# Kernel tuning notes

Measured on AMD Instinct MI355X. Metric: run time of the kernel, lower is better.

## Reference

```python
import jax, jax.numpy as jnp
import numpy as np

N = 16384          # tokens
D_IN = 512         # input_dim
D_OUT = 512        # output_dim
H = 256            # expert hidden
E = 10             # num_experts
TOP_K = 2


def setup_inputs() -> dict:
    key = jax.random.key(0)
    ks = jax.random.split(key, 12)
    s_in = 1.0 / np.sqrt(D_IN)
    s_h = 1.0 / np.sqrt(H)
    s_o = 1.0 / np.sqrt(D_OUT)
    return {
        "x": jax.random.normal(ks[0], (N, D_IN), dtype=jnp.float32),
        "gate_w": jax.random.uniform(ks[1], (D_IN, E), minval=-s_in, maxval=s_in),
        "gate_b": jax.random.uniform(ks[2], (E,), minval=-s_in, maxval=s_in),
        "w1": jax.random.uniform(ks[3], (E, D_IN, H), minval=-s_in, maxval=s_in),
        "b1": jax.random.uniform(ks[4], (E, H), minval=-s_in, maxval=s_in),
        "w2": jax.random.uniform(ks[5], (E, H, D_OUT), minval=-s_h, maxval=s_h),
        "b2": jax.random.uniform(ks[6], (E, D_OUT), minval=-s_h, maxval=s_h),
        "cls_w": jax.random.uniform(ks[7], (D_OUT, D_OUT), minval=-s_o, maxval=s_o),
        "cls_b": jax.random.uniform(ks[8], (D_OUT,), minval=-s_o, maxval=s_o),
        "vec_w": jax.random.uniform(ks[9], (D_OUT, D_OUT), minval=-s_o, maxval=s_o),
        "vec_b": jax.random.uniform(ks[10], (D_OUT,), minval=-s_o, maxval=s_o),
    }


def reference(x, gate_w, gate_b, w1, b1, w2, b2, cls_w, cls_b, vec_w, vec_b):
    # Gating: softmax over experts, take top-k, renormalize
    gate_probs = jax.nn.softmax(x @ gate_w + gate_b, axis=-1)          # [N, E]
    top_v, top_i = jax.lax.top_k(gate_probs, TOP_K)                    # [N, K]
    top_v = top_v / jnp.sum(top_v, axis=-1, keepdims=True)
    # Scatter renormalized top-k probs into dense per-expert weights [N, E]
    n_idx = jnp.arange(x.shape[0])[:, None]
    w = jnp.zeros_like(gate_probs).at[n_idx, top_i].add(top_v)
    # Expert MLPs (vectorized over experts; zero weight == not dispatched)
    h = jax.nn.relu(jnp.einsum("nd,edh->neh", x, w1) + b1)             # [N, E, H]
    y = jnp.einsum("neh,eho->neo", h, w2) + b2                          # [N, E, Dout]
    combined = jnp.einsum("neo,ne->no", y, w)                           # [N, Dout]
    cls_out = combined @ cls_w + cls_b
    vec_out = combined @ vec_w + vec_b
    return (cls_out, vec_out)
```

## Files before the change

kernel.cpp:

```cpp
#include <hip/hip_runtime.h>

#define NTOK 16384
#define DIN  512
#define DOUT 512
#define HDIM 256
#define NEXP 10
#define NSLOT (2*NTOK)
#define NSEG  (2*NEXP)
#define BM 128
#define BN 128
#define BK 64

typedef unsigned short u16;
typedef unsigned int   u32;
typedef short s16x8 __attribute__((ext_vector_type(8)));
typedef float f32x4 __attribute__((ext_vector_type(4)));

__device__ __forceinline__ u16 f2b(float f){
  union { float f; u32 u; } c; c.f = f;
  u32 r = c.u + 0x7FFFu + ((c.u >> 16) & 1u);
  return (u16)(r >> 16);
}
__device__ __forceinline__ float b2f(u16 v){
  union { u32 u; float f; } c; c.u = ((u32)v) << 16; return c.f;
}
__device__ __forceinline__ u32 pk2(float lo, float hi){
  u32 r;
  asm("v_cvt_pk_bf16_f32 %0, %1, %2" : "=v"(r) : "v"(lo), "v"(hi));
  return r;
}
__device__ __forceinline__ s16x8 cvt8(const float* p){
  f32x4 a = *(const f32x4*)p;
  f32x4 b = *(const f32x4*)(p + 4);
  union { u32 u[4]; s16x8 v; } c;
  c.u[0] = pk2(a[0], a[1]); c.u[1] = pk2(a[2], a[3]);
  c.u[2] = pk2(b[0], b[1]); c.u[3] = pk2(b[2], b[3]);
  return c.v;
}

__global__ __launch_bounds__(64) void k_zero(int* counts){
  if (threadIdx.x < NSEG) counts[threadIdx.x] = 0;
}

__global__ __launch_bounds__(256) void k_gate(
    const float* __restrict__ x, const float* __restrict__ gw, const float* __restrict__ gb,
    int* __restrict__ tke, float* __restrict__ tkw, int* __restrict__ counts)
{
  __shared__ int cnt[NSEG];
  __shared__ __align__(16) float xs[16*512];
  __shared__ __align__(16) float lgw[5120];
  const int tid = threadIdx.x;
  if (tid < NSEG) cnt[tid] = 0;
  for (int d = tid; d < 512; d += 256){
    float g[10];
    #pragma unroll
    for (int r = 0; r < 10; ++r) g[r] = gw[d*10 + r];
    #pragma unroll
    for (int p = 0; p < 5; ++p){
      lgw[(p*512 + d)*2    ] = g[2*p];
      lgw[(p*512 + d)*2 + 1] = g[2*p+1];
    }
  }
  const float* xsrc = x + (size_t)blockIdx.x * 16 * 512;
  #pragma unroll
  for (int q = 0; q < 8; ++q){
    int i = tid + q*256;
    *(f32x4*)&xs[i*4] = *(const f32x4*)&xsrc[i*4];
  }
  __syncthreads();

  const int wave = tid >> 6, lane = tid & 63;
  #pragma unroll
  for (int tt = 0; tt < 4; ++tt){
    const int lt = wave*4 + tt;
    const int token = blockIdx.x*16 + lt;
    float acc[NEXP];
    #pragma unroll
    for (int e = 0; e < NEXP; ++e) acc[e] = 0.f;
    #pragma unroll
    for (int dd = 0; dd < 8; ++dd){
      int d = dd*64 + lane;
      float xv = xs[lt*512 + d];
      #pragma unroll
      for (int p = 0; p < 5; ++p){
        float2 g2 = *(const float2*)&lgw[(p*512 + d)*2];
        acc[2*p]   += xv * g2.x;
        acc[2*p+1] += xv * g2.y;
      }
    }
    #pragma unroll
    for (int e = 0; e < NEXP; ++e){
      #pragma unroll
      for (int off = 32; off > 0; off >>= 1) acc[e] += __shfl_xor(acc[e], off, 64);
    }
    if (lane == 0){
      float l[NEXP];
      #pragma unroll
      for (int e = 0; e < NEXP; ++e) l[e] = acc[e] + gb[e];
      int bi = 0; float bv = l[0];
      #pragma unroll
      for (int e = 1; e < NEXP; ++e) if (l[e] > bv){ bv = l[e]; bi = e; }
      int si = -1; float sv = -1e30f;
      #pragma unroll
      for (int e = 0; e < NEXP; ++e) if (e != bi && l[e] > sv){ sv = l[e]; si = e; }
      float w0 = 1.f / (1.f + expf(sv - bv));
      tke[2*token]   = bi;  tke[2*token+1] = si;
      tkw[2*token]   = w0;  tkw[2*token+1] = 1.f - w0;
      atomicAdd(&cnt[2*bi], 1);  atomicAdd(&cnt[2*si+1], 1);
    }
  }
  __syncthreads();
  if (tid < NSEG && cnt[tid] > 0)
    atomicAdd(&counts[tid], cnt[tid]);
}

__global__ __launch_bounds__(64) void k_scan(
    const int* __restrict__ counts, int* __restrict__ offsets, int* __restrict__ cursors)
{
  if (threadIdx.x == 0){
    int s = 0;
    for (int i = 0; i < NSEG; ++i){ offsets[i] = s; s += counts[i]; }
    offsets[NSEG] = s;
  }
  if (threadIdx.x < NSEG) cursors[threadIdx.x] = 0;
}

__global__ __launch_bounds__(256) void k_scatter(
    const int* __restrict__ tke, const float* __restrict__ tkw,
    const int* __restrict__ offsets, int* __restrict__ cursors,
    int* __restrict__ tok_slot, float* __restrict__ w_slot)
{
  __shared__ int lcnt[NSEG], lbase[NSEG];
  if (threadIdx.x < NSEG) lcnt[threadIdx.x] = 0;
  __syncthreads();
  int n = blockIdx.x * 256 + threadIdx.x;
  int g0 = 2*tke[2*n], g1 = 2*tke[2*n+1] + 1;
  int p0 = atomicAdd(&lcnt[g0], 1);
  int p1 = atomicAdd(&lcnt[g1], 1);
  __syncthreads();
  if (threadIdx.x < NSEG) lbase[threadIdx.x] = atomicAdd(&cursors[threadIdx.x], lcnt[threadIdx.x]);
  __syncthreads();
  int s0 = offsets[g0] + lbase[g0] + p0;
  int s1 = offsets[g1] + lbase[g1] + p1;
  tok_slot[s0] = n; w_slot[s0] = tkw[2*n];
  tok_slot[s1] = n; w_slot[s1] = tkw[2*n+1];
}

__global__ __launch_bounds__(256) void k_wt(
    const float* __restrict__ in, u16* __restrict__ out, int R, int C)
{
  __shared__ float tile[32][33];
  const float* src = in + (size_t)blockIdx.z * R * C;
  u16* dst = out + (size_t)blockIdx.z * R * C;
  int cb = blockIdx.x * 32, rb = blockIdx.y * 32;
  int tx = threadIdx.x & 31, ty = threadIdx.x >> 5;
  #pragma unroll
  for (int i = 0; i < 4; ++i)
    tile[ty + i*8][tx] = src[(size_t)(rb + ty + i*8) * C + cb + tx];
  __syncthreads();
  #pragma unroll
  for (int i = 0; i < 4; ++i)
    dst[(size_t)(cb + ty + i*8) * R + rb + tx] = f2b(tile[tx][ty + i*8]);
}

__global__ __launch_bounds__(256) void k_wtt(
    const float* __restrict__ W, u16* __restrict__ out)
{
  int gid = blockIdx.x * 256 + threadIdx.x;
  int c16 = gid & 15;
  int kc  = (gid >> 4) & 63;
  int cg  = gid >> 10;
  int col = cg*16 + c16;
  s16x8 v;
  #pragma unroll
  for (int q = 0; q < 8; ++q)
    v[q] = (short)f2b(W[(size_t)(kc*8 + q) * DOUT + col]);
  *(s16x8*)(out + (size_t)gid * 8) = v;
}

__global__ __launch_bounds__(256, 2) void k_h(
    const float* __restrict__ x, const u16* __restrict__ w1tb, const float* __restrict__ b1,
    const int* __restrict__ offsets, const int* __restrict__ tok_slot,
    u16* __restrict__ h)
{
  __shared__ __align__(16) char pool[65536];
  u16* As = (u16*)pool;
  u16* Bs = (u16*)(pool + 32768);
  __shared__ int toks[BM];
  const int e   = blockIdx.z;
  const int off = offsets[2*e];
  const int cnt = offsets[2*e+2] - off;
  const int c0  = blockIdx.x * BM;
  if (c0 >= cnt) return;
  const int n0  = blockIdx.y * BN;
  const int tid = threadIdx.x;

  if (tid < BM){
    int r = c0 + tid;
    toks[tid] = tok_slot[off + (r < cnt ? r : cnt - 1)];
  }
  __syncthreads();

  const u16* Bg = w1tb + ((size_t)e * HDIM + n0) * DIN;

  int crow[4], ckk[4];
  #pragma unroll
  for (int i = 0; i < 4; ++i){
    int c = tid + i*256;
    crow[i] = c >> 3; ckk[i] = (c & 7) * 8;
  }
  int tokr[4];
  #pragma unroll
  for (int i = 0; i < 4; ++i) tokr[i] = toks[crow[i]];

  s16x8 ra[4], rb[4];
  auto loadregs = [&](int ks){
    #pragma unroll
    for (int i = 0; i < 4; ++i){
      ra[i] = cvt8(x + (size_t)tokr[i]*DIN + ks*BK + ckk[i]);
      rb[i] = *(const s16x8*)(Bg + (size_t)crow[i]*DIN + ks*BK + ckk[i]);
    }
  };
  auto writeregs = [&](int buf){
    #pragma unroll
    for (int i = 0; i < 4; ++i){
      u32 byt = (u32)((crow[i]*BK + ckk[i])*2) ^ ((u32)(crow[i]&7)<<4);
      *(s16x8*)((char*)As + buf*16384 + byt) = ra[i];
      *(s16x8*)((char*)Bs + buf*16384 + byt) = rb[i];
    }
  };

  const int wv = tid >> 6, lane = tid & 63;
  const int lr = lane & 15, lk = lane >> 4;
  const int wr = (wv >> 1) * 64, wc = (wv & 1) * 64;

  f32x4 acc[4][4];
  #pragma unroll
  for (int i = 0; i < 4; ++i)
    #pragma unroll
    for (int j = 0; j < 4; ++j) acc[i][j] = (f32x4){0.f,0.f,0.f,0.f};

  loadregs(0); writeregs(0);
  int cur = 0;
  const int NK = DIN / BK;
  for (int ks = 0; ks < NK; ++ks){
    __syncthreads();
    if (ks + 1 < NK) loadregs(ks + 1);
    #pragma unroll
    for (int sub = 0; sub < 2; ++sub){
      s16x8 af[4], bf[4];
      #pragma unroll
      for (int g = 0; g < 4; ++g){
        int arow = wr + g*16 + lr;
        u32 ab = (u32)((arow*BK + sub*32 + lk*8)*2) ^ ((u32)(arow&7)<<4);
        af[g] = *(const s16x8*)((char*)As + cur*16384 + ab);
        int bcol = wc + g*16 + lr;
        u32 bb = (u32)((bcol*BK + sub*32 + lk*8)*2) ^ ((u32)(bcol&7)<<4);
        bf[g] = *(const s16x8*)((char*)Bs + cur*16384 + bb);
      }
      #pragma unroll
      for (int i = 0; i < 4; ++i)
        #pragma unroll
        for (int j = 0; j < 4; ++j)
          acc[i][j] = __builtin_amdgcn_mfma_f32_16x16x32_bf16(af[i], bf[j], acc[i][j], 0, 0, 0);
    }
    if (ks + 1 < NK) writeregs(cur ^ 1);
    cur ^= 1;
  }
  __syncthreads();

  u16* outh = (u16*)pool;
  #pragma unroll
  for (int j = 0; j < 4; ++j){
    int col = wc + j*16 + lr;
    float bias = b1[e*HDIM + n0 + col];
    #pragma unroll
    for (int i = 0; i < 4; ++i)
      #pragma unroll
      for (int r = 0; r < 4; ++r){
        int row = wr + i*16 + lk*4 + r;
        float v = acc[i][j][r] + bias;
        outh[row*136 + col] = f2b(v > 0.f ? v : 0.f);
      }
  }
  __syncthreads();
  {
    int r = tid >> 1, half = tid & 1;
    if (c0 + r < cnt){
      u16* dst = h + (size_t)(off + c0 + r) * HDIM + n0 + half*64;
      const u16* src = outh + r*136 + half*64;
      #pragma unroll
      for (int q = 0; q < 8; ++q)
        *(s16x8*)(dst + q*8) = *(const s16x8*)(src + q*8);
    }
  }
}

template<int PASS>
__global__ __launch_bounds__(256, 2) void k_y(
    const u16* __restrict__ h, const u16* __restrict__ w2tb, const float* __restrict__ b2,
    const int* __restrict__ offsets, const int* __restrict__ tok_slot,
    const float* __restrict__ w_slot, u16* __restrict__ cmb)
{
  __shared__ __align__(16) char pool[67584];
  u16* As = (u16*)pool;
  u16* Bs = (u16*)(pool + 32768);
  __shared__ int   toks[BM];
  __shared__ float wts[BM];
  const int e    = blockIdx.z;
  const int segb = offsets[2*e + PASS];
  const int segc = offsets[2*e + PASS + 1] - segb;
  const int c0   = blockIdx.x * BM;
  if (c0 >= segc) return;
  const int n0   = blockIdx.y * BN;
  const int tid  = threadIdx.x;

  if (tid < BM){
    int r = c0 + tid;
    int s = segb + (r < segc ? r : segc - 1);
    toks[tid] = tok_slot[s];
    wts[tid]  = w_slot[s];
  }

  const u16* Ag = h + (size_t)(segb + c0) * HDIM;
  const u16* Bg = w2tb + ((size_t)e * DOUT + n0) * HDIM;

  int crow[4], ckk[4];
  #pragma unroll
  for (int i = 0; i < 4; ++i){
    int c = tid + i*256;
    crow[i] = c >> 3; ckk[i] = (c & 7) * 8;
  }
  s16x8 ra[4], rb[4];
  auto loadregs = [&](int ks){
    #pragma unroll
    for (int i = 0; i < 4; ++i){
      ra[i] = *(const s16x8*)(Ag + (size_t)crow[i]*HDIM + ks*BK + ckk[i]);
      rb[i] = *(const s16x8*)(Bg + (size_t)crow[i]*HDIM + ks*BK + ckk[i]);
    }
  };
  auto writeregs = [&](int buf){
    #pragma unroll
    for (int i = 0; i < 4; ++i){
      u32 byt = (u32)((crow[i]*BK + ckk[i])*2) ^ ((u32)(crow[i]&7)<<4);
      *(s16x8*)((char*)As + buf*16384 + byt) = ra[i];
      *(s16x8*)((char*)Bs + buf*16384 + byt) = rb[i];
    }
  };

  const int wv = tid >> 6, lane = tid & 63;
  const int lr = lane & 15, lk = lane >> 4;
  const int wr = (wv >> 1) * 64, wc = (wv & 1) * 64;

  f32x4 acc[4][4];
  #pragma unroll
  for (int i = 0; i < 4; ++i)
    #pragma unroll
    for (int j = 0; j < 4; ++j) acc[i][j] = (f32x4){0.f,0.f,0.f,0.f};

  loadregs(0); writeregs(0);
  int cur = 0;
  const int NK = HDIM / BK;
  for (int ks = 0; ks < NK; ++ks){
    __syncthreads();
    if (ks + 1 < NK) loadregs(ks + 1);
    #pragma unroll
    for (int sub = 0; sub < 2; ++sub){
      s16x8 af[4], bf[4];
      #pragma unroll
      for (int g = 0; g < 4; ++g){
        int arow = wr + g*16 + lr;
        u32 ab = (u32)((arow*BK + sub*32 + lk*8)*2) ^ ((u32)(arow&7)<<4);
        af[g] = *(const s16x8*)((char*)As + cur*16384 + ab);
        int bcol = wc + g*16 + lr;
        u32 bb = (u32)((bcol*BK + sub*32 + lk*8)*2) ^ ((u32)(bcol&7)<<4);
        bf[g] = *(const s16x8*)((char*)Bs + cur*16384 + bb);
      }
      #pragma unroll
      for (int i = 0; i < 4; ++i)
        #pragma unroll
        for (int j = 0; j < 4; ++j)
          acc[i][j] = __builtin_amdgcn_mfma_f32_16x16x32_bf16(af[i], bf[j], acc[i][j], 0, 0, 0);
    }
    if (ks + 1 < NK) writeregs(cur ^ 1);
    cur ^= 1;
  }
  __syncthreads();

  float* outf = (float*)pool;
  #pragma unroll
  for (int j = 0; j < 4; ++j){
    int col = wc + j*16 + lr;
    float bias = b2[e*DOUT + n0 + col];
    #pragma unroll
    for (int i = 0; i < 4; ++i)
      #pragma unroll
      for (int r = 0; r < 4; ++r){
        int row = wr + i*16 + lk*4 + r;
        outf[row*132 + col] = wts[row] * (acc[i][j][r] + bias);
      }
  }
  __syncthreads();
  {
    int r = tid >> 1, half = tid & 1;
    if (c0 + r < segc){
      u16* dst = cmb + (size_t)toks[r] * 1024 + n0 + half*64;
      const float* src = outf + r*132 + half*64;
      #pragma unroll
      for (int q = 0; q < 8; ++q){
        s16x8 o;
        if (PASS == 0){
          #pragma unroll
          for (int m = 0; m < 8; ++m) o[m] = (short)f2b(src[q*8 + m]);
        } else {
          s16x8 old = *(const s16x8*)(dst + q*8);
          #pragma unroll
          for (int m = 0; m < 8; ++m)
            o[m] = (short)f2b(b2f((u16)old[m]) + src[q*8 + m]);
        }
        *(s16x8*)(dst + q*8) = o;
      }
    }
  }
}

__global__ __launch_bounds__(512, 4) void k_cls(
    const u16* __restrict__ cmb, const float* __restrict__ W,
    const float* __restrict__ bias, float* __restrict__ out)
{
  __shared__ __align__(16) char Bs[2][10240];
  const int tid = threadIdx.x;
  const int r0  = blockIdx.x * 256;
  const int c0  = blockIdx.y * 128;

  const int bc4 = tid >> 4;
  const int bkp = tid & 15;
  u32 bpk[4];
  auto loadB = [&](int ks){
    const float* p0 = W + (size_t)(ks*32 + 2*bkp) * DOUT + c0 + bc4*4;
    f32x4 v0 = *(const f32x4*)p0;
    f32x4 v1 = *(const f32x4*)(p0 + DOUT);
    #pragma unroll
    for (int m = 0; m < 4; ++m) bpk[m] = pk2(v0[m], v1[m]);
  };
  auto writeB = [&](int buf){
    #pragma unroll
    for (int m = 0; m < 4; ++m)
      *(u32*)(Bs[buf] + (bc4*4 + m)*80 + bkp*4) = bpk[m];
  };

  const int wv = tid >> 6, lane = tid & 63;
  const int lr = lane & 15, lk = lane >> 4;
  const int rg = wv >> 1, cg = wv & 1;
  const u16* Arow = cmb + (size_t)(r0 + rg*64) * 1024;

  f32x4 acc[4][4];
  #pragma unroll
  for (int i = 0; i < 4; ++i)
    #pragma unroll
    for (int j = 0; j < 4; ++j) acc[i][j] = (f32x4){0.f,0.f,0.f,0.f};

  s16x8 af[4], afn[4];
  auto loadA = [&](s16x8* a, int ks){
    #pragma unroll
    for (int g = 0; g < 4; ++g)
      a[g] = *(const s16x8*)(Arow + (size_t)(g*16 + lr)*1024 + ks*32 + lk*8);
  };

  loadB(0); writeB(0); loadA(af, 0);
  int cur = 0;
  for (int ks = 0; ks < 16; ++ks){
    __syncthreads();
    if (ks + 1 < 16){ loadB(ks + 1); loadA(afn, ks + 1); }
    s16x8 bf[4];
    #pragma unroll
    for (int j = 0; j < 4; ++j)
      bf[j] = *(const s16x8*)(Bs[cur] + (cg*64 + j*16 + lr)*80 + lk*16);
    #pragma unroll
    for (int i = 0; i < 4; ++i)
      #pragma unroll
      for (int j = 0; j < 4; ++j)
        acc[i][j] = __builtin_amdgcn_mfma_f32_16x16x32_bf16(af[i], bf[j], acc[i][j], 0, 0, 0);
    if (ks + 1 < 16) writeB(cur ^ 1);
    #pragma unroll
    for (int g = 0; g < 4; ++g) af[g] = afn[g];
    cur ^= 1;
  }

  #pragma unroll
  for (int j = 0; j < 4; ++j){
    int col = c0 + cg*64 + j*16 + lr;
    float bv = bias[col];
    #pragma unroll
    for (int i = 0; i < 4; ++i)
      #pragma unroll
      for (int r = 0; r < 4; ++r){
        int row = r0 + rg*64 + i*16 + lk*4 + r;
        out[(size_t)row * DOUT + col] = acc[i][j][r] + bv;
      }
  }
}

__global__ __launch_bounds__(512, 2) void k_vip(
    const float* __restrict__ W, const float* __restrict__ bias,
    u16* __restrict__ cmbio)
{
  __shared__ __align__(16) char Bs[2][40960];
  const int tid = threadIdx.x;
  const int r0  = blockIdx.x * 64;

  int bc4[4], bkp[4];
  #pragma unroll
  for (int u = 0; u < 4; ++u){
    int idx = tid + u*512;
    bc4[u] = idx >> 4;
    bkp[u] = idx & 15;
  }
  u32 bpk[4][4];
  auto loadB = [&](int ks){
    #pragma unroll
    for (int u = 0; u < 4; ++u){
      const float* p0 = W + (size_t)(ks*32 + 2*bkp[u]) * DOUT + bc4[u]*4;
      f32x4 v0 = *(const f32x4*)p0;
      f32x4 v1 = *(const f32x4*)(p0 + DOUT);
      #pragma unroll
      for (int m = 0; m < 4; ++m) bpk[u][m] = pk2(v0[m], v1[m]);
    }
  };
  auto writeB = [&](int buf){
    #pragma unroll
    for (int u = 0; u < 4; ++u)
      #pragma unroll
      for (int m = 0; m < 4; ++m)
        *(u32*)(Bs[buf] + (bc4[u]*4 + m)*80 + bkp[u]*4) = bpk[u][m];
  };

  const int wv = tid >> 6, lane = tid & 63;
  const int lr = lane & 15, lk = lane >> 4;
  const int wc = wv * 64;
  const u16* Arow = cmbio + (size_t)r0 * 1024;

  f32x4 acc[4][4];
  #pragma unroll
  for (int i = 0; i < 4; ++i)
    #pragma unroll
    for (int j = 0; j < 4; ++j) acc[i][j] = (f32x4){0.f,0.f,0.f,0.f};

  s16x8 af[4], afn[4];
  auto loadA = [&](s16x8* a, int ks){
    #pragma unroll
    for (int g = 0; g < 4; ++g)
      a[g] = *(const s16x8*)(Arow + (size_t)(g*16 + lr)*1024 + ks*32 + lk*8);
  };

  loadB(0); writeB(0); loadA(af, 0);
  int cur = 0;
  for (int ks = 0; ks < 16; ++ks){
    __syncthreads();
    if (ks + 1 < 16){ loadB(ks + 1); loadA(afn, ks + 1); }
    s16x8 bf[4];
    #pragma unroll
    for (int g = 0; g < 4; ++g)
      bf[g] = *(const s16x8*)(Bs[cur] + (wc + g*16 + lr)*80 + lk*16);
    #pragma unroll
    for (int i = 0; i < 4; ++i)
      #pragma unroll
      for (int j = 0; j < 4; ++j)
        acc[i][j] = __builtin_amdgcn_mfma_f32_16x16x32_bf16(af[i], bf[j], acc[i][j], 0, 0, 0);
    if (ks + 1 < 16) writeB(cur ^ 1);
    #pragma unroll
    for (int g = 0; g < 4; ++g) af[g] = afn[g];
    cur ^= 1;
  }
  __syncthreads();

  float* out = (float*)cmbio;
  #pragma unroll
  for (int j = 0; j < 4; ++j){
    int col = wc + j*16 + lr;
    float bv = bias[col];
    #pragma unroll
    for (int i = 0; i < 4; ++i)
      #pragma unroll
      for (int r = 0; r < 4; ++r){
        int row = r0 + i*16 + lk*4 + r;
        out[(size_t)row * DOUT + col] = acc[i][j][r] + bv;
      }
  }
}

__global__ __launch_bounds__(256, 2) void k_vipw(
    const u16* __restrict__ wTt, const float* __restrict__ bias,
    u16* __restrict__ cmbio)
{
  const int tid = threadIdx.x;
  const int r0  = blockIdx.x * 32;
  const int wv = tid >> 6, lane = tid & 63;
  const int lr = lane & 15, lk = lane >> 4;
  const int wc = wv * 128;
  const int cg0 = wv * 8;
  const u16* Arow = cmbio + (size_t)r0 * 1024;

  f32x4 acc[2][8];
  #pragma unroll
  for (int i = 0; i < 2; ++i)
    #pragma unroll
    for (int j = 0; j < 8; ++j) acc[i][j] = (f32x4){0.f,0.f,0.f,0.f};

  s16x8 a0[2], b0[8], a1[2], b1[8];
  auto loadA = [&](s16x8* a, int ks){
    #pragma unroll
    for (int g = 0; g < 2; ++g)
      a[g] = *(const s16x8*)(Arow + (size_t)(g*16 + lr)*1024 + ks*32 + lk*8);
  };
  auto loadB = [&](s16x8* b, int ks){
    #pragma unroll
    for (int j = 0; j < 8; ++j){
      int chunk = (cg0 + j)*64 + ks*4 + lk;
      b[j] = *(const s16x8*)(wTt + (size_t)chunk*128 + lr*8);
    }
  };
  auto step = [&](const s16x8* a, const s16x8* b){
    #pragma unroll
    for (int j = 0; j < 8; ++j)
      #pragma unroll
      for (int i = 0; i < 2; ++i)
        acc[i][j] = __builtin_amdgcn_mfma_f32_16x16x32_bf16(a[i], b[j], acc[i][j], 0, 0, 0);
  };

  loadA(a0, 0); loadB(b0, 0);
  #pragma unroll
  for (int ks = 0; ks < 16; ks += 2){
    if (ks + 1 < 16){ loadA(a1, ks + 1); loadB(b1, ks + 1); }
    step(a0, b0);
    if (ks + 2 < 16){ loadA(a0, ks + 2); loadB(b0, ks + 2); }
    step(a1, b1);
  }
  __syncthreads();

  float* out = (float*)cmbio;
  #pragma unroll
  for (int j = 0; j < 8; ++j){
    int col = wc + j*16 + lr;
    float bv = bias[col];
    #pragma unroll
    for (int i = 0; i < 2; ++i)
      #pragma unroll
      for (int r = 0; r < 4; ++r){
        int row = r0 + i*16 + lk*4 + r;
        out[(size_t)row * DOUT + col] = acc[i][j][r] + bv;
      }
  }
}

extern "C" void kernel_launch(void* const* d_in, const int* in_sizes, int n_in,
                              void* d_out, int out_size, void* d_ws, size_t ws_size,
                              hipStream_t stream)
{
  const float* x    = (const float*)d_in[0];
  const float* gw   = (const float*)d_in[1];
  const float* gb   = (const float*)d_in[2];
  const float* w1   = (const float*)d_in[3];
  const float* b1   = (const float*)d_in[4];
  const float* w2   = (const float*)d_in[5];
  const float* b2   = (const float*)d_in[6];
  const float* clsw = (const float*)d_in[7];
  const float* clsb = (const float*)d_in[8];
  const float* vecw = (const float*)d_in[9];
  const float* vecb = (const float*)d_in[10];

  char* base = (char*)d_out;
  float* cls_out  = (float*)base;
  u16*   cmb      = (u16*)(base + ((size_t)32<<20));
  u16*   h        = (u16*)base;
  char*  mb       = base + ((size_t)16<<20) + (128<<10);
  int*   tok_slot = (int*)  mb;
  float* w_slot   = (float*)(mb + 131072);
  int*   tke      = (int*)  (mb + 262144);
  float* tkw      = (float*)(mb + 393216);
  int*   counts   = (int*)  (mb + 524288);
  int*   offsets  = (int*)  (mb + 524544);
  int*   cursors  = (int*)  (mb + 524800);
  u16*   w1tb     = (u16*)(base + ((size_t)18<<20));
  u16*   w2tb     = (u16*)(base + ((size_t)21<<20));

  const bool usews = (ws_size >= (size_t)(1<<20));
  u16* vecwTt = (u16*)d_ws;

  k_zero<<<dim3(1), dim3(64), 0, stream>>>(counts);
  k_gate<<<dim3(NTOK/16), dim3(256), 0, stream>>>(x, gw, gb, tke, tkw, counts);
  k_scan<<<dim3(1), dim3(64), 0, stream>>>(counts, offsets, cursors);
  k_scatter<<<dim3(NTOK/256), dim3(256), 0, stream>>>(tke, tkw, offsets, cursors,
                                                      tok_slot, w_slot);
  k_wt<<<dim3(HDIM/32, DIN/32, NEXP), dim3(256), 0, stream>>>(w1, w1tb, DIN, HDIM);
  k_wt<<<dim3(DOUT/32, HDIM/32, NEXP), dim3(256), 0, stream>>>(w2, w2tb, HDIM, DOUT);
  if (usews)
    k_wtt<<<dim3(128), dim3(256), 0, stream>>>(vecw, vecwTt);
  k_h<<<dim3(256, 2, NEXP), dim3(256), 0, stream>>>(x, w1tb, b1, offsets, tok_slot, h);
  k_y<0><<<dim3(128, 4, NEXP), dim3(256), 0, stream>>>(h, w2tb, b2, offsets, tok_slot, w_slot, cmb);
  k_y<1><<<dim3(128, 4, NEXP), dim3(256), 0, stream>>>(h, w2tb, b2, offsets, tok_slot, w_slot, cmb);
  k_cls<<<dim3(NTOK/256, DOUT/128), dim3(512), 0, stream>>>(cmb, clsw, clsb, cls_out);
  if (usews)
    k_vipw<<<dim3(NTOK/32), dim3(256), 0, stream>>>(vecwTt, vecb, cmb);
  else
    k_vip<<<dim3(NTOK/64), dim3(512), 0, stream>>>(vecw, vecb, cmb);
}
```

Measured before the change: 204.8 us.

## Prepack expert weights in MFMA fragment layout and read B directly from global

Expert weights w1 and w2 are now converted into a fragment-tiled bf16 layout, so each lane's B operand for the MFMA is one contiguous 16-byte load from global memory. The B tile no longer goes through LDS, which roughly halves shared memory per block and lets launch bounds rise to 3 blocks per CU. The k_y epilogue now stages bf16 instead of fp32 in LDS. This trades LDS traffic and barriers for per-iteration global (L2-cached) weight loads in the inner loop, whose latency is no longer hidden by the double buffer. A single generic prepack kernel also replaces the two earlier transpose kernels.

Measured after the change: 203.7 us (median of 4 runs). Within noise of the previous version (-0.6%).

```diff
diff --git a/kernel.cpp b/kernel.cpp
--- a/kernel.cpp
+++ b/kernel.cpp
@@ -146,53 +146,39 @@
   tok_slot[s1] = n; w_slot[s1] = tkw[2*n+1];
 }
 
-__global__ __launch_bounds__(256) void k_wt(
-    const float* __restrict__ in, u16* __restrict__ out, int R, int C)
-{
-  __shared__ float tile[32][33];
-  const float* src = in + (size_t)blockIdx.z * R * C;
-  u16* dst = out + (size_t)blockIdx.z * R * C;
-  int cb = blockIdx.x * 32, rb = blockIdx.y * 32;
-  int tx = threadIdx.x & 31, ty = threadIdx.x >> 5;
-  #pragma unroll
-  for (int i = 0; i < 4; ++i)
-    tile[ty + i*8][tx] = src[(size_t)(rb + ty + i*8) * C + cb + tx];
-  __syncthreads();
-  #pragma unroll
-  for (int i = 0; i < 4; ++i)
-    dst[(size_t)(cb + ty + i*8) * R + rb + tx] = f2b(tile[tx][ty + i*8]);
-}
-
-__global__ __launch_bounds__(256) void k_wtt(
-    const float* __restrict__ W, u16* __restrict__ out)
-{
-  int gid = blockIdx.x * 256 + threadIdx.x;
-  int c16 = gid & 15;
-  int kc  = (gid >> 4) & 63;
-  int cg  = gid >> 10;
-  int col = cg*16 + c16;
+__global__ __launch_bounds__(256) void k_wtf(
+    const float* __restrict__ W, u16* __restrict__ out, int KC8, int C16)
+{
+  const int e   = blockIdx.z;
+  const int gid = blockIdx.x * 256 + threadIdx.x;
+  const int c16 = gid & 15;
+  const int rem = gid >> 4;
+  const int kc  = rem % KC8;
+  const int cg  = rem / KC8;
+  const int K = KC8 * 8, C = C16 * 16;
+  const float* src = W + (size_t)e*K*C + (size_t)(kc*8)*C + cg*16 + c16;
   s16x8 v;
   #pragma unroll
   for (int q = 0; q < 8; ++q)
-    v[q] = (short)f2b(W[(size_t)(kc*8 + q) * DOUT + col]);
-  *(s16x8*)(out + (size_t)gid * 8) = v;
-}
-
-__global__ __launch_bounds__(256, 2) void k_h(
-    const float* __restrict__ x, const u16* __restrict__ w1tb, const float* __restrict__ b1,
+    v[q] = (short)f2b(src[(size_t)q * C]);
+  size_t t = ((size_t)e*C16 + cg)*KC8 + kc;
+  *(s16x8*)(out + t*128 + c16*8) = v;
+}
+
+__global__ __launch_bounds__(256, 3) void k_h(
+    const float* __restrict__ x, const u16* __restrict__ w1f, const float* __restrict__ b1,
     const int* __restrict__ offsets, const int* __restrict__ tok_slot,
     u16* __restrict__ h)
 {
-  __shared__ __align__(16) char pool[65536];
+  __shared__ __align__(16) char pool[34816];
   u16* As = (u16*)pool;
-  u16* Bs = (u16*)(pool + 32768);
   __shared__ int toks[BM];
   const int e   = blockIdx.z;
+  const int hh  = blockIdx.y;
   const int off = offsets[2*e];
   const int cnt = offsets[2*e+2] - off;
   const int c0  = blockIdx.x * BM;
   if (c0 >= cnt) return;
-  const int n0  = blockIdx.y * BN;
   const int tid = threadIdx.x;
 
   if (tid < BM){
@@ -201,8 +187,6 @@
   }
   __syncthreads();
 
-  const u16* Bg = w1tb + ((size_t)e * HDIM + n0) * DIN;
-
   int crow[4], ckk[4];
   #pragma unroll
   for (int i = 0; i < 4; ++i){
@@ -213,26 +197,24 @@
   #pragma unroll
   for (int i = 0; i < 4; ++i) tokr[i] = toks[crow[i]];
 
-  s16x8 ra[4], rb[4];
+  s16x8 ra[4];
   auto loadregs = [&](int ks){
     #pragma unroll
-    for (int i = 0; i < 4; ++i){
+    for (int i = 0; i < 4; ++i)
       ra[i] = cvt8(x + (size_t)tokr[i]*DIN + ks*BK + ckk[i]);
-      rb[i] = *(const s16x8*)(Bg + (size_t)crow[i]*DIN + ks*BK + ckk[i]);
-    }
   };
   auto writeregs = [&](int buf){
     #pragma unroll
     for (int i = 0; i < 4; ++i){
       u32 byt = (u32)((crow[i]*BK + ckk[i])*2) ^ ((u32)(crow[i]&7)<<4);
       *(s16x8*)((char*)As + buf*16384 + byt) = ra[i];
-      *(s16x8*)((char*)Bs + buf*16384 + byt) = rb[i];
     }
   };
 
   const int wv = tid >> 6, lane = tid & 63;
   const int lr = lane & 15, lk = lane >> 4;
   const int wr = (wv >> 1) * 64, wc = (wv & 1) * 64;
+  const int cgb = e*16 + hh*8 + (wv & 1)*4;
 
   f32x4 acc[4][4];
   #pragma unroll
@@ -248,15 +230,14 @@
     if (ks + 1 < NK) loadregs(ks + 1);
     #pragma unroll
     for (int sub = 0; sub < 2; ++sub){
+      int kc = ks*8 + sub*4 + lk;
       s16x8 af[4], bf[4];
       #pragma unroll
       for (int g = 0; g < 4; ++g){
         int arow = wr + g*16 + lr;
         u32 ab = (u32)((arow*BK + sub*32 + lk*8)*2) ^ ((u32)(arow&7)<<4);
         af[g] = *(const s16x8*)((char*)As + cur*16384 + ab);
-        int bcol = wc + g*16 + lr;
-        u32 bb = (u32)((bcol*BK + sub*32 + lk*8)*2) ^ ((u32)(bcol&7)<<4);
-        bf[g] = *(const s16x8*)((char*)Bs + cur*16384 + bb);
+        bf[g] = *(const s16x8*)(w1f + ((size_t)(cgb + g)*64 + kc)*128 + lr*8);
       }
       #pragma unroll
       for (int i = 0; i < 4; ++i)
@@ -270,6 +251,7 @@
   __syncthreads();
 
   u16* outh = (u16*)pool;
+  const int n0 = hh * 128;
   #pragma unroll
   for (int j = 0; j < 4; ++j){
     int col = wc + j*16 + lr;
@@ -297,22 +279,22 @@
 }
 
 template<int PASS>
-__global__ __launch_bounds__(256, 2) void k_y(
-    const u16* __restrict__ h, const u16* __restrict__ w2tb, const float* __restrict__ b2,
+__global__ __launch_bounds__(256, 3) void k_y(
+    const u16* __restrict__ h, const u16* __restrict__ w2f, const float* __restrict__ b2,
     const int* __restrict__ offsets, const int* __restrict__ tok_slot,
     const float* __restrict__ w_slot, u16* __restrict__ cmb)
 {
-  __shared__ __align__(16) char pool[67584];
+  __shared__ __align__(16) char pool[34816];
   u16* As = (u16*)pool;
-  u16* Bs = (u16*)(pool + 32768);
   __shared__ int   toks[BM];
   __shared__ float wts[BM];
   const int e    = blockIdx.z;
+  const int q4   = blockIdx.y;
   const int segb = offsets[2*e + PASS];
   const int segc = offsets[2*e + PASS + 1] - segb;
   const int c0   = blockIdx.x * BM;
   if (c0 >= segc) return;
-  const int n0   = blockIdx.y * BN;
+  const int n0   = q4 * BN;
   const int tid  = threadIdx.x;
 
   if (tid < BM){
@@ -321,9 +303,9 @@
     toks[tid] = tok_slot[s];
     wts[tid]  = w_slot[s];
   }
+  __syncthreads();
 
   const u16* Ag = h + (size_t)(segb + c0) * HDIM;
-  const u16* Bg = w2tb + ((size_t)e * DOUT + n0) * HDIM;
 
   int crow[4], ckk[4];
   #pragma unroll
@@ -331,26 +313,24 @@
     int c = tid + i*256;
     crow[i] = c >> 3; ckk[i] = (c & 7) * 8;
   }
-  s16x8 ra[4], rb[4];
+  s16x8 ra[4];
   auto loadregs = [&](int ks){
     #pragma unroll
-    for (int i = 0; i < 4; ++i){
+    for (int i = 0; i < 4; ++i)
       ra[i] = *(const s16x8*)(Ag + (size_t)crow[i]*HDIM + ks*BK + ckk[i]);
-      rb[i] = *(const s16x8*)(Bg + (size_t)crow[i]*HDIM + ks*BK + ckk[i]);
-    }
   };
   auto writeregs = [&](int buf){
     #pragma unroll
     for (int i = 0; i < 4; ++i){
       u32 byt = (u32)((crow[i]*BK + ckk[i])*2) ^ ((u32)(crow[i]&7)<<4);
       *(s16x8*)((char*)As + buf*16384 + byt) = ra[i];
-      *(s16x8*)((char*)Bs + buf*16384 + byt) = rb[i];
     }
   };
 
   const int wv = tid >> 6, lane = tid & 63;
   const int lr = lane & 15, lk = lane >> 4;
   const int wr = (wv >> 1) * 64, wc = (wv & 1) * 64;
+  const int cgb = e*32 + q4*8 + (wv & 1)*4;
 
   f32x4 acc[4][4];
   #pragma unroll
@@ -366,15 +346,14 @@
     if (ks + 1 < NK) loadregs(ks + 1);
     #pragma unroll
     for (int sub = 0; sub < 2; ++sub){
+      int kc = ks*8 + sub*4 + lk;
       s16x8 af[4], bf[4];
       #pragma unroll
       for (int g = 0; g < 4; ++g){
         int arow = wr + g*16 + lr;
         u32 ab = (u32)((arow*BK + sub*32 + lk*8)*2) ^ ((u32)(arow&7)<<4);
         af[g] = *(const s16x8*)((char*)As + cur*16384 + ab);
-        int bcol = wc + g*16 + lr;
-        u32 bb = (u32)((bcol*BK + sub*32 + lk*8)*2) ^ ((u32)(bcol&7)<<4);
-        bf[g] = *(const s16x8*)((char*)Bs + cur*16384 + bb);
+        bf[g] = *(const s16x8*)(w2f + ((size_t)(cgb + g)*32 + kc)*128 + lr*8);
       }
       #pragma unroll
       for (int i = 0; i < 4; ++i)
@@ -387,7 +366,7 @@
   }
   __syncthreads();
 
-  float* outf = (float*)pool;
+  u16* outh = (u16*)pool;
   #pragma unroll
   for (int j = 0; j < 4; ++j){
     int col = wc + j*16 + lr;
@@ -397,7 +376,7 @@
       #pragma unroll
       for (int r = 0; r < 4; ++r){
         int row = wr + i*16 + lk*4 + r;
-        outf[row*132 + col] = wts[row] * (acc[i][j][r] + bias);
+        outh[row*136 + col] = f2b(wts[row] * (acc[i][j][r] + bias));
       }
   }
   __syncthreads();
@@ -405,20 +384,17 @@
     int r = tid >> 1, half = tid & 1;
     if (c0 + r < segc){
       u16* dst = cmb + (size_t)toks[r] * 1024 + n0 + half*64;
-      const float* src = outf + r*132 + half*64;
+      const u16* src = outh + r*136 + half*64;
       #pragma unroll
       for (int q = 0; q < 8; ++q){
-        s16x8 o;
-        if (PASS == 0){
-          #pragma unroll
-          for (int m = 0; m < 8; ++m) o[m] = (short)f2b(src[q*8 + m]);
-        } else {
+        s16x8 s = *(const s16x8*)(src + q*8);
+        if (PASS == 1){
           s16x8 old = *(const s16x8*)(dst + q*8);
           #pragma unroll
           for (int m = 0; m < 8; ++m)
-            o[m] = (short)f2b(b2f((u16)old[m]) + src[q*8 + m]);
+            s[m] = (short)f2b(b2f((u16)old[m]) + b2f((u16)s[m]));
         }
-        *(s16x8*)(dst + q*8) = o;
+        *(s16x8*)(dst + q*8) = s;
       }
     }
   }
@@ -681,8 +657,8 @@
   int*   counts   = (int*)  (mb + 524288);
   int*   offsets  = (int*)  (mb + 524544);
   int*   cursors  = (int*)  (mb + 524800);
-  u16*   w1tb     = (u16*)(base + ((size_t)18<<20));
-  u16*   w2tb     = (u16*)(base + ((size_t)21<<20));
+  u16*   w1f      = (u16*)(base + ((size_t)18<<20));
+  u16*   w2f      = (u16*)(base + ((size_t)21<<20));
 
   const bool usews = (ws_size >= (size_t)(1<<20));
   u16* vecwTt = (u16*)d_ws;
@@ -692,13 +668,13 @@
   k_scan<<<dim3(1), dim3(64), 0, stream>>>(counts, offsets, cursors);
   k_scatter<<<dim3(NTOK/256), dim3(256), 0, stream>>>(tke, tkw, offsets, cursors,
                                                       tok_slot, w_slot);
-  k_wt<<<dim3(HDIM/32, DIN/32, NEXP), dim3(256), 0, stream>>>(w1, w1tb, DIN, HDIM);
-  k_wt<<<dim3(DOUT/32, HDIM/32, NEXP), dim3(256), 0, stream>>>(w2, w2tb, HDIM, DOUT);
+  k_wtf<<<dim3(64, 1, NEXP), dim3(256), 0, stream>>>(w1, w1f, 64, 16);
+  k_wtf<<<dim3(64, 1, NEXP), dim3(256), 0, stream>>>(w2, w2f, 32, 32);
   if (usews)
-    k_wtt<<<dim3(128), dim3(256), 0, stream>>>(vecw, vecwTt);
-  k_h<<<dim3(256, 2, NEXP), dim3(256), 0, stream>>>(x, w1tb, b1, offsets, tok_slot, h);
-  k_y<0><<<dim3(128, 4, NEXP), dim3(256), 0, stream>>>(h, w2tb, b2, offsets, tok_slot, w_slot, cmb);
-  k_y<1><<<dim3(128, 4, NEXP), dim3(256), 0, stream>>>(h, w2tb, b2, offsets, tok_slot, w_slot, cmb);
+    k_wtf<<<dim3(128, 1, 1), dim3(256), 0, stream>>>(vecw, vecwTt, 64, 32);
+  k_h<<<dim3(256, 2, NEXP), dim3(256), 0, stream>>>(x, w1f, b1, offsets, tok_slot, h);
+  k_y<0><<<dim3(128, 4, NEXP), dim3(256), 0, stream>>>(h, w2f, b2, offsets, tok_slot, w_slot, cmb);
+  k_y<1><<<dim3(128, 4, NEXP), dim3(256), 0, stream>>>(h, w2f, b2, offsets, tok_slot, w_slot, cmb);
   k_cls<<<dim3(NTOK/256, DOUT/128), dim3(512), 0, stream>>>(cmb, clsw, clsb, cls_out);
   if (usews)
     k_vipw<<<dim3(NTOK/32), dim3(256), 0, stream>>>(vecwTt, vecb, cmb);
```
